# Optimization experiments

Measured on AMD Instinct MI355X. Metric: run time of the kernel, lower is better.

## Reference

```python
import jax, jax.numpy as jnp
import numpy as np

BATCH, H, NFAM = 32768, 1024, 10


def setup_inputs() -> dict:
    key = jax.random.key(0)
    k1, k2, k3, k4 = jax.random.split(key, 4)
    scale1 = 1.0 / np.sqrt(2 * H)
    scale2 = 1.0 / np.sqrt(H)
    return {
        "features": jax.random.normal(k1, (BATCH, H), dtype=jnp.float32),
        "prototypes": jax.random.normal(k2, (NFAM, H), dtype=jnp.float32),
        "W1": jax.random.normal(k3, (2 * H, H), dtype=jnp.float32) * scale1,
        "b1": jnp.zeros((H,), dtype=jnp.float32),
        "W2": jax.random.normal(k4, (H, H), dtype=jnp.float32) * scale2,
        "b2": jnp.zeros((H,), dtype=jnp.float32),
    }


def reference(features, prototypes, W1, b1, W2, b2):
    # Squared euclidean distances via the norm trick (avoids [B, NFAM, H] blowup).
    # argmin over squared distances == argmin over cdist (sqrt is monotone).
    f2 = jnp.sum(features * features, axis=1, keepdims=True)        # [B, 1]
    p2 = jnp.sum(prototypes * prototypes, axis=1)                   # [NFAM]
    d2 = f2 + p2[None, :] - 2.0 * (features @ prototypes.T)         # [B, NFAM]
    nearest_idx = jnp.argmin(d2, axis=1)                            # [B]
    nearest_prototypes = prototypes[nearest_idx]                    # [B, H]
    combined = jnp.concatenate([features, nearest_prototypes], axis=1)  # [B, 2H]
    hidden = jax.nn.relu(combined @ W1 + b1)                        # [B, H]
    adapted = hidden @ W2 + b2                                      # [B, H]
    return adapted
```

## Files before the change

### kernel.cpp

```cpp
#include <hip/hip_runtime.h>
#include <stdint.h>
#include <stddef.h>

#define BATCH 32768
#define HDIM  1024
#define NFAM  10

typedef short bf16x8 __attribute__((ext_vector_type(8)));
typedef float f32x4  __attribute__((ext_vector_type(4)));

__device__ __forceinline__ unsigned short f2bf(float x) {
  unsigned int u = __builtin_bit_cast(unsigned int, x);
  u += 0x7fffu + ((u >> 16) & 1u);
  return (unsigned short)(u >> 16);
}

__device__ __forceinline__ void async_cp16(unsigned short* lds_dst, const unsigned short* g_src) {
  __builtin_amdgcn_global_load_lds(
      (const __attribute__((address_space(1))) unsigned int*)g_src,
      (__attribute__((address_space(3))) unsigned int*)lds_dst,
      16, 0, 0);
}

__global__ __launch_bounds__(256) void transpose_cast(
    const float* __restrict__ in, unsigned short* __restrict__ out, int R, int C) {
  __shared__ float tile[64][65];
  const int t = threadIdx.x;
  const int c = t & 63;
  const int r0 = t >> 6;
  const int rbase = blockIdx.y * 64, cbase = blockIdx.x * 64;
#pragma unroll
  for (int i = 0; i < 16; ++i) {
    int r = r0 + i * 4;
    tile[r][c] = in[(size_t)(rbase + r) * C + cbase + c];
  }
  __syncthreads();
#pragma unroll
  for (int i = 0; i < 16; ++i) {
    int r = r0 + i * 4;
    out[(size_t)(cbase + r) * R + rbase + c] = f2bf(tile[c][r]);
  }
}

__global__ __launch_bounds__(256) void proto_prep(
    const float* __restrict__ protos, float* __restrict__ p2) {
  __shared__ float red[4];
  const int j = blockIdx.x, t = threadIdx.x;
  float4 v = ((const float4*)(protos + (size_t)j * HDIM))[t];
  float s = v.x * v.x + v.y * v.y + v.z * v.z + v.w * v.w;
#pragma unroll
  for (int o = 32; o > 0; o >>= 1) s += __shfl_down(s, o);
  if ((t & 63) == 0) red[t >> 6] = s;
  __syncthreads();
  if (t == 0) p2[j] = red[0] + red[1] + red[2] + red[3];
}

__global__ __launch_bounds__(256) void proto_contrib(
    const float* __restrict__ protos, const float* __restrict__ W1,
    const float* __restrict__ b1, float* __restrict__ protoC) {
  __shared__ float red[4][64];
  const int j  = blockIdx.y;
  const int ln = threadIdx.x & 63;
  const int ks = threadIdx.x >> 6;
  const int n  = blockIdx.x * 64 + ln;
  const float* p = protos + (size_t)j * HDIM + ks * 256;
  const float* w = W1 + (size_t)(HDIM + ks * 256) * HDIM + n;
  float s = 0.f;
#pragma unroll 16
  for (int kk = 0; kk < 256; ++kk)
    s += p[kk] * w[(size_t)kk * HDIM];
  red[ks][ln] = s;
  __syncthreads();
  if (ks == 0)
    protoC[j * HDIM + n] = red[0][ln] + red[1][ln] + red[2][ln] + red[3][ln] + b1[n];
}

__global__ __launch_bounds__(256) void nearest_kernel(
    const float* __restrict__ feats, const float* __restrict__ protos,
    const float* __restrict__ p2, unsigned short* __restrict__ featsB,
    int* __restrict__ idx) {
  __shared__ float pl[NFAM * HDIM];
  const int t = threadIdx.x;
#pragma unroll
  for (int j = 0; j < NFAM; ++j)
    ((float4*)pl)[t + 256 * j] = ((const float4*)protos)[t + 256 * j];
  __syncthreads();

  const int wave = t >> 6, lane = t & 63;
  float P2[NFAM];
#pragma unroll
  for (int j = 0; j < NFAM; ++j) P2[j] = p2[j];

#pragma unroll
  for (int rr = 0; rr < 4; ++rr) {
    const int row = blockIdx.x * 16 + wave * 4 + rr;
    const float* f = feats + (size_t)row * HDIM;

    float dot[NFAM];
#pragma unroll
    for (int j = 0; j < NFAM; ++j) dot[j] = 0.f;
    float f2 = 0.f;

#pragma unroll
    for (int ch = 0; ch < 4; ++ch) {
      const int k4 = ch * 64 + lane;
      float4 v = ((const float4*)f)[k4];
      f2 += v.x * v.x + v.y * v.y + v.z * v.z + v.w * v.w;
#pragma unroll
      for (int j = 0; j < NFAM; ++j) {
        float4 p = ((const float4*)pl)[j * 256 + k4];
        dot[j] += v.x * p.x + v.y * p.y + v.z * p.z + v.w * p.w;
      }
      uint2 pk;
      pk.x = (unsigned)f2bf(v.x) | ((unsigned)f2bf(v.y) << 16);
      pk.y = (unsigned)f2bf(v.z) | ((unsigned)f2bf(v.w) << 16);
      *(uint2*)(featsB + (size_t)row * HDIM + k4 * 4) = pk;
    }

#pragma unroll
    for (int o = 32; o > 0; o >>= 1) {
      f2 += __shfl_down(f2, o);
#pragma unroll
      for (int j = 0; j < NFAM; ++j) dot[j] += __shfl_down(dot[j], o);
    }
    if (lane == 0) {
      int best = 0;
      float bd = f2 + P2[0] - 2.f * dot[0];
#pragma unroll
      for (int j = 1; j < NFAM; ++j) {
        float d = f2 + P2[j] - 2.f * dot[j];
        if (d < bd) { bd = d; best = j; }
      }
      idx[row] = best;
    }
  }
}

template <int EPI>
__global__ __launch_bounds__(512, 2) void gemm256(
    const unsigned short* __restrict__ A,
    const unsigned short* __restrict__ Bt,
    const int* __restrict__ idx,
    const float* __restrict__ protoC,
    const float* __restrict__ bias,
    unsigned short* __restrict__ outB,
    float* __restrict__ outF) {
  constexpr int K  = 1024;
  constexpr int NT = K / 64;
  __shared__ unsigned short ldsA[2 * 2 * 2 * 128 * 32];
  __shared__ unsigned short ldsB[2 * 2 * 2 * 128 * 32];

  const int t    = threadIdx.x;
  const int lane = t & 63;
  const int quad = lane >> 4;
  const int r16  = lane & 15;
  const int wid  = t >> 6;
  const int wm   = wid >> 2;
  const int wn   = wid & 3;

  const int b = blockIdx.x;
  const int rowBase = ((b >> 5) + (b & 7) * 16) * 256;
  const int colBase = ((b >> 3) & 3) * 256;

  const int sr = t >> 2;
  const int q  = (t & 3) ^ ((t >> 3) & 3);
  const unsigned short* pA = A  + (size_t)(rowBase + sr) * K + q * 8;
  const unsigned short* pB = Bt + (size_t)(colBase + sr) * K + q * 8;
  const int ldst = t * 8;

  const int pr = quad ^ ((r16 >> 1) & 3);

  f32x4 acc[2][2][4][2];
#pragma unroll
  for (int a0 = 0; a0 < 2; ++a0)
#pragma unroll
    for (int b0 = 0; b0 < 2; ++b0)
#pragma unroll
      for (int m0 = 0; m0 < 4; ++m0)
#pragma unroll
        for (int n0 = 0; n0 < 2; ++n0) acc[a0][b0][m0][n0] = (f32x4){0.f, 0.f, 0.f, 0.f};

#define STAGE_A(buf, h, kb)                                                        \
  {                                                                                \
    async_cp16(ldsA + (buf) * 16384 + (0 * 2 + (h)) * 4096 + ldst,                 \
               pA + (size_t)(h) * (128 * K) + (kb) + 0 * 32);                      \
    async_cp16(ldsA + (buf) * 16384 + (1 * 2 + (h)) * 4096 + ldst,                 \
               pA + (size_t)(h) * (128 * K) + (kb) + 1 * 32);                      \
  }
#define STAGE_B(buf, h, kb)                                                        \
  {                                                                                \
    async_cp16(ldsB + (buf) * 16384 + (0 * 2 + (h)) * 4096 + ldst,                 \
               pB + (size_t)(h) * (128 * K) + (kb) + 0 * 32);                      \
    async_cp16(ldsB + (buf) * 16384 + (1 * 2 + (h)) * 4096 + ldst,                 \
               pB + (size_t)(h) * (128 * K) + (kb) + 1 * 32);                      \
  }
#define READ_A(dst, p_, h)                                                          \
  _Pragma("unroll")                                                                 \
  for (int s = 0; s < 2; ++s)                                                       \
    _Pragma("unroll")                                                               \
    for (int mi = 0; mi < 4; ++mi)                                                  \
      dst[s][mi] = *(const bf16x8*)(ldsA + (p_) * 16384 + (s * 2 + (h)) * 4096 +    \
                                    (wm * 64 + mi * 16 + r16) * 32 + pr * 8);
#define READ_B(dst, p_, h)                                                          \
  _Pragma("unroll")                                                                 \
  for (int s = 0; s < 2; ++s)                                                       \
    _Pragma("unroll")                                                               \
    for (int ni = 0; ni < 2; ++ni)                                                  \
      dst[s][ni] = *(const bf16x8*)(ldsB + (p_) * 16384 + (s * 2 + (h)) * 4096 +    \
                                    (wn * 32 + ni * 16 + r16) * 32 + pr * 8);
#define MFMA_Q(ah, bh, bsrc)                                                        \
  __builtin_amdgcn_s_setprio(1);                                                    \
  _Pragma("unroll")                                                                 \
  for (int s = 0; s < 2; ++s)                                                       \
    _Pragma("unroll")                                                               \
    for (int mi = 0; mi < 4; ++mi)                                                  \
      _Pragma("unroll")                                                             \
      for (int ni = 0; ni < 2; ++ni)                                                \
        acc[ah][bh][mi][ni] = __builtin_amdgcn_mfma_f32_16x16x32_bf16(              \
            av[s][mi], bsrc[s][ni], acc[ah][bh][mi][ni], 0, 0, 0);                  \
  __builtin_amdgcn_s_setprio(0);

  STAGE_A(0, 0, 0);
  STAGE_B(0, 1, 0);
  STAGE_A(0, 1, 0);
  STAGE_B(0, 0, 0);
  STAGE_A(1, 0, 64);
  STAGE_B(1, 1, 64);
  asm volatile("s_waitcnt vmcnt(4)" ::: "memory");
  __builtin_amdgcn_s_barrier();

  bf16x8 av[2][4], bvlo[2][2], bvhi[2][2];

  for (int kt = 0; kt < NT; ++kt) {
    const int p   = kt & 1;
    const int kb1 = ((kt + 1) & (NT - 1)) * 64;
    const int kb2 = ((kt + 2) & (NT - 1)) * 64;

    READ_A(av, p, 0);
    READ_B(bvlo, p, 0);
    STAGE_A(p ^ 1, 1, kb1);
    __builtin_amdgcn_s_barrier();
    MFMA_Q(0, 0, bvlo);
    __builtin_amdgcn_s_barrier();

    READ_B(bvhi, p, 1);
    STAGE_B(p ^ 1, 0, kb1);
    __builtin_amdgcn_s_barrier();
    MFMA_Q(0, 1, bvhi);
    __builtin_amdgcn_s_barrier();

    READ_A(av, p, 1);
    STAGE_A(p, 0, kb2);
    __builtin_amdgcn_s_barrier();
    MFMA_Q(1, 1, bvhi);
    __builtin_amdgcn_s_barrier();

    STAGE_B(p, 1, kb2);
    asm volatile("s_waitcnt vmcnt(4)" ::: "memory");
    __builtin_amdgcn_s_barrier();
    MFMA_Q(1, 0, bvlo);
    __builtin_amdgcn_s_barrier();
  }
#undef STAGE_A
#undef STAGE_B
#undef READ_A
#undef READ_B
#undef MFMA_Q

#pragma unroll
  for (int ah = 0; ah < 2; ++ah) {
#pragma unroll
    for (int mi = 0; mi < 4; ++mi) {
      const int grow0 = rowBase + ah * 128 + wm * 64 + mi * 16 + quad * 4;
      int pid[4];
      if (EPI) {
#pragma unroll
        for (int r = 0; r < 4; ++r) pid[r] = idx[grow0 + r];
      }
#pragma unroll
      for (int bh = 0; bh < 2; ++bh) {
#pragma unroll
        for (int ni = 0; ni < 2; ++ni) {
          const int gcol = colBase + bh * 128 + wn * 32 + ni * 16 + r16;
          if (EPI) {
#pragma unroll
            for (int r = 0; r < 4; ++r) {
              float v = acc[ah][bh][mi][ni][r] + protoC[(size_t)pid[r] * HDIM + gcol];
              v = fmaxf(v, 0.0f);
              outB[(size_t)(grow0 + r) * 1024 + gcol] = f2bf(v);
            }
          } else {
            const float bv = bias[gcol];
#pragma unroll
            for (int r = 0; r < 4; ++r)
              outF[(size_t)(grow0 + r) * 1024 + gcol] = acc[ah][bh][mi][ni][r] + bv;
          }
        }
      }
    }
  }
}

extern "C" void kernel_launch(void* const* d_in, const int* in_sizes, int n_in,
                              void* d_out, int out_size, void* d_ws, size_t ws_size,
                              hipStream_t stream) {
  const float* feats  = (const float*)d_in[0];
  const float* protos = (const float*)d_in[1];
  const float* W1     = (const float*)d_in[2];
  const float* b1     = (const float*)d_in[3];
  const float* W2     = (const float*)d_in[4];
  const float* b2     = (const float*)d_in[5];
  float* out = (float*)d_out;

  unsigned short* featsB  = (unsigned short*)d_ws;
  unsigned short* hiddenB = featsB + (size_t)BATCH * HDIM;
  unsigned short* W1t     = hiddenB + (size_t)BATCH * HDIM;
  unsigned short* W2t     = W1t + (size_t)HDIM * HDIM;
  float* protoC = (float*)(W2t + (size_t)HDIM * HDIM);
  float* p2     = protoC + NFAM * HDIM;
  int* idx      = (int*)(p2 + NFAM + 2);

  transpose_cast<<<dim3(HDIM / 64, HDIM / 64), 256, 0, stream>>>(W1, W1t, HDIM, HDIM);
  transpose_cast<<<dim3(HDIM / 64, HDIM / 64), 256, 0, stream>>>(W2, W2t, HDIM, HDIM);
  proto_prep<<<NFAM, 256, 0, stream>>>(protos, p2);
  proto_contrib<<<dim3(HDIM / 64, NFAM), 256, 0, stream>>>(protos, W1, b1, protoC);
  nearest_kernel<<<BATCH / 16, 256, 0, stream>>>(feats, protos, p2, featsB, idx);
  gemm256<1><<<512, 512, 0, stream>>>(featsB, W1t, idx, protoC, nullptr, hiddenB, nullptr);
  gemm256<0><<<512, 512, 0, stream>>>(hiddenB, W2t, nullptr, nullptr, b2, nullptr, out);
}
```

Baseline: 413.2 us.

## Merge five preprocessing kernels into one block-dispatched prep kernel

The two weight transpose-casts, prototype norm, prototype contribution and nearest-prototype kernels are merged into a single launch whose block index selects the role. Prototype squared norms are now computed redundantly inside each nearest block from LDS rather than by a separate kernel. This removes four launches and the serialization between independent small kernels, letting them overlap. In exchange, every block reserves the 40KB LDS sized for the largest role, which can reduce occupancy for the transpose and contrib blocks, and each nearest block does some extra reduction work.

Result: faster. 398.3 us (-3.6%).

```diff
diff --git a/kernel.cpp b/kernel.cpp
--- a/kernel.cpp
+++ b/kernel.cpp
@@ -22,117 +22,126 @@
       16, 0, 0);
 }
 
-__global__ __launch_bounds__(256) void transpose_cast(
-    const float* __restrict__ in, unsigned short* __restrict__ out, int R, int C) {
-  __shared__ float tile[64][65];
+#define NEAREST_BLKS  2048
+#define TR1_BASE      2048
+#define TR2_BASE      2304
+#define CONTRIB_BASE  2560
+#define PREP_BLKS     2720
+
+__global__ __launch_bounds__(256) void prep_kernel(
+    const float* __restrict__ feats, const float* __restrict__ protos,
+    const float* __restrict__ W1, const float* __restrict__ b1,
+    const float* __restrict__ W2,
+    unsigned short* __restrict__ featsB, int* __restrict__ idx,
+    float* __restrict__ protoC,
+    unsigned short* __restrict__ W1t, unsigned short* __restrict__ W2t) {
+  __shared__ __align__(16) char smem[40960];
+  const int b = blockIdx.x;
   const int t = threadIdx.x;
-  const int c = t & 63;
-  const int r0 = t >> 6;
-  const int rbase = blockIdx.y * 64, cbase = blockIdx.x * 64;
-#pragma unroll
-  for (int i = 0; i < 16; ++i) {
-    int r = r0 + i * 4;
-    tile[r][c] = in[(size_t)(rbase + r) * C + cbase + c];
-  }
-  __syncthreads();
-#pragma unroll
-  for (int i = 0; i < 16; ++i) {
-    int r = r0 + i * 4;
-    out[(size_t)(cbase + r) * R + rbase + c] = f2bf(tile[c][r]);
-  }
-}
-
-__global__ __launch_bounds__(256) void proto_prep(
-    const float* __restrict__ protos, float* __restrict__ p2) {
-  __shared__ float red[4];
-  const int j = blockIdx.x, t = threadIdx.x;
-  float4 v = ((const float4*)(protos + (size_t)j * HDIM))[t];
-  float s = v.x * v.x + v.y * v.y + v.z * v.z + v.w * v.w;
-#pragma unroll
-  for (int o = 32; o > 0; o >>= 1) s += __shfl_down(s, o);
-  if ((t & 63) == 0) red[t >> 6] = s;
-  __syncthreads();
-  if (t == 0) p2[j] = red[0] + red[1] + red[2] + red[3];
-}
-
-__global__ __launch_bounds__(256) void proto_contrib(
-    const float* __restrict__ protos, const float* __restrict__ W1,
-    const float* __restrict__ b1, float* __restrict__ protoC) {
-  __shared__ float red[4][64];
-  const int j  = blockIdx.y;
-  const int ln = threadIdx.x & 63;
-  const int ks = threadIdx.x >> 6;
-  const int n  = blockIdx.x * 64 + ln;
-  const float* p = protos + (size_t)j * HDIM + ks * 256;
-  const float* w = W1 + (size_t)(HDIM + ks * 256) * HDIM + n;
-  float s = 0.f;
+
+  if (b < NEAREST_BLKS) {
+    float* pl = (float*)smem;
+#pragma unroll
+    for (int j = 0; j < NFAM; ++j)
+      ((float4*)pl)[t + 256 * j] = ((const float4*)protos)[t + 256 * j];
+    __syncthreads();
+
+    const int wave = t >> 6, lane = t & 63;
+
+    float P2[NFAM];
+#pragma unroll
+    for (int j = 0; j < NFAM; ++j) {
+      float s = 0.f;
+#pragma unroll
+      for (int c = 0; c < 4; ++c) {
+        float4 v = ((const float4*)pl)[j * 256 + c * 64 + lane];
+        s += v.x * v.x + v.y * v.y + v.z * v.z + v.w * v.w;
+      }
+#pragma unroll
+      for (int o = 32; o > 0; o >>= 1) s += __shfl_down(s, o);
+      P2[j] = s;
+    }
+
+#pragma unroll
+    for (int rr = 0; rr < 4; ++rr) {
+      const int row = b * 16 + wave * 4 + rr;
+      const float* f = feats + (size_t)row * HDIM;
+
+      float dot[NFAM];
+#pragma unroll
+      for (int j = 0; j < NFAM; ++j) dot[j] = 0.f;
+      float f2 = 0.f;
+
+#pragma unroll
+      for (int ch = 0; ch < 4; ++ch) {
+        const int k4 = ch * 64 + lane;
+        float4 v = ((const float4*)f)[k4];
+        f2 += v.x * v.x + v.y * v.y + v.z * v.z + v.w * v.w;
+#pragma unroll
+        for (int j = 0; j < NFAM; ++j) {
+          float4 p = ((const float4*)pl)[j * 256 + k4];
+          dot[j] += v.x * p.x + v.y * p.y + v.z * p.z + v.w * p.w;
+        }
+        uint2 pk;
+        pk.x = (unsigned)f2bf(v.x) | ((unsigned)f2bf(v.y) << 16);
+        pk.y = (unsigned)f2bf(v.z) | ((unsigned)f2bf(v.w) << 16);
+        *(uint2*)(featsB + (size_t)row * HDIM + k4 * 4) = pk;
+      }
+
+#pragma unroll
+      for (int o = 32; o > 0; o >>= 1) {
+        f2 += __shfl_down(f2, o);
+#pragma unroll
+        for (int j = 0; j < NFAM; ++j) dot[j] += __shfl_down(dot[j], o);
+      }
+      if (lane == 0) {
+        int best = 0;
+        float bd = f2 + P2[0] - 2.f * dot[0];
+#pragma unroll
+        for (int j = 1; j < NFAM; ++j) {
+          float d = f2 + P2[j] - 2.f * dot[j];
+          if (d < bd) { bd = d; best = j; }
+        }
+        idx[row] = best;
+      }
+    }
+  } else if (b < CONTRIB_BASE) {
+    const int bi = (b < TR2_BASE) ? (b - TR1_BASE) : (b - TR2_BASE);
+    const float* in = (b < TR2_BASE) ? W1 : W2;
+    unsigned short* out = (b < TR2_BASE) ? W1t : W2t;
+    float (*tile)[65] = (float(*)[65])smem;
+    const int c = t & 63;
+    const int r0 = t >> 6;
+    const int rbase = (bi >> 4) * 64, cbase = (bi & 15) * 64;
+#pragma unroll
+    for (int i = 0; i < 16; ++i) {
+      int r = r0 + i * 4;
+      tile[r][c] = in[(size_t)(rbase + r) * HDIM + cbase + c];
+    }
+    __syncthreads();
+#pragma unroll
+    for (int i = 0; i < 16; ++i) {
+      int r = r0 + i * 4;
+      out[(size_t)(cbase + r) * HDIM + rbase + c] = f2bf(tile[c][r]);
+    }
+  } else {
+    float (*red)[64] = (float(*)[64])smem;
+    const int bi = b - CONTRIB_BASE;
+    const int j  = bi >> 4;
+    const int nc = bi & 15;
+    const int ln = t & 63;
+    const int ks = t >> 6;
+    const int n  = nc * 64 + ln;
+    const float* p = protos + (size_t)j * HDIM + ks * 256;
+    const float* w = W1 + (size_t)(HDIM + ks * 256) * HDIM + n;
+    float s = 0.f;
 #pragma unroll 16
-  for (int kk = 0; kk < 256; ++kk)
-    s += p[kk] * w[(size_t)kk * HDIM];
-  red[ks][ln] = s;
-  __syncthreads();
-  if (ks == 0)
-    protoC[j * HDIM + n] = red[0][ln] + red[1][ln] + red[2][ln] + red[3][ln] + b1[n];
-}
-
-__global__ __launch_bounds__(256) void nearest_kernel(
-    const float* __restrict__ feats, const float* __restrict__ protos,
-    const float* __restrict__ p2, unsigned short* __restrict__ featsB,
-    int* __restrict__ idx) {
-  __shared__ float pl[NFAM * HDIM];
-  const int t = threadIdx.x;
-#pragma unroll
-  for (int j = 0; j < NFAM; ++j)
-    ((float4*)pl)[t + 256 * j] = ((const float4*)protos)[t + 256 * j];
-  __syncthreads();
-
-  const int wave = t >> 6, lane = t & 63;
-  float P2[NFAM];
-#pragma unroll
-  for (int j = 0; j < NFAM; ++j) P2[j] = p2[j];
-
-#pragma unroll
-  for (int rr = 0; rr < 4; ++rr) {
-    const int row = blockIdx.x * 16 + wave * 4 + rr;
-    const float* f = feats + (size_t)row * HDIM;
-
-    float dot[NFAM];
-#pragma unroll
-    for (int j = 0; j < NFAM; ++j) dot[j] = 0.f;
-    float f2 = 0.f;
-
-#pragma unroll
-    for (int ch = 0; ch < 4; ++ch) {
-      const int k4 = ch * 64 + lane;
-      float4 v = ((const float4*)f)[k4];
-      f2 += v.x * v.x + v.y * v.y + v.z * v.z + v.w * v.w;
-#pragma unroll
-      for (int j = 0; j < NFAM; ++j) {
-        float4 p = ((const float4*)pl)[j * 256 + k4];
-        dot[j] += v.x * p.x + v.y * p.y + v.z * p.z + v.w * p.w;
-      }
-      uint2 pk;
-      pk.x = (unsigned)f2bf(v.x) | ((unsigned)f2bf(v.y) << 16);
-      pk.y = (unsigned)f2bf(v.z) | ((unsigned)f2bf(v.w) << 16);
-      *(uint2*)(featsB + (size_t)row * HDIM + k4 * 4) = pk;
-    }
-
-#pragma unroll
-    for (int o = 32; o > 0; o >>= 1) {
-      f2 += __shfl_down(f2, o);
-#pragma unroll
-      for (int j = 0; j < NFAM; ++j) dot[j] += __shfl_down(dot[j], o);
-    }
-    if (lane == 0) {
-      int best = 0;
-      float bd = f2 + P2[0] - 2.f * dot[0];
-#pragma unroll
-      for (int j = 1; j < NFAM; ++j) {
-        float d = f2 + P2[j] - 2.f * dot[j];
-        if (d < bd) { bd = d; best = j; }
-      }
-      idx[row] = best;
-    }
+    for (int kk = 0; kk < 256; ++kk)
+      s += p[kk] * w[(size_t)kk * HDIM];
+    red[ks][ln] = s;
+    __syncthreads();
+    if (ks == 0)
+      protoC[j * HDIM + n] = red[0][ln] + red[1][ln] + red[2][ln] + red[3][ln] + b1[n];
   }
 }
 
@@ -317,14 +326,10 @@
   unsigned short* W1t     = hiddenB + (size_t)BATCH * HDIM;
   unsigned short* W2t     = W1t + (size_t)HDIM * HDIM;
   float* protoC = (float*)(W2t + (size_t)HDIM * HDIM);
-  float* p2     = protoC + NFAM * HDIM;
-  int* idx      = (int*)(p2 + NFAM + 2);
-
-  transpose_cast<<<dim3(HDIM / 64, HDIM / 64), 256, 0, stream>>>(W1, W1t, HDIM, HDIM);
-  transpose_cast<<<dim3(HDIM / 64, HDIM / 64), 256, 0, stream>>>(W2, W2t, HDIM, HDIM);
-  proto_prep<<<NFAM, 256, 0, stream>>>(protos, p2);
-  proto_contrib<<<dim3(HDIM / 64, NFAM), 256, 0, stream>>>(protos, W1, b1, protoC);
-  nearest_kernel<<<BATCH / 16, 256, 0, stream>>>(feats, protos, p2, featsB, idx);
+  int* idx      = (int*)(protoC + NFAM * HDIM);
+
+  prep_kernel<<<PREP_BLKS, 256, 0, stream>>>(
+      feats, protos, W1, b1, W2, featsB, idx, protoC, W1t, W2t);
   gemm256<1><<<512, 512, 0, stream>>>(featsB, W1t, idx, protoC, nullptr, hiddenB, nullptr);
   gemm256<0><<<512, 512, 0, stream>>>(hiddenB, W2t, nullptr, nullptr, b2, nullptr, out);
 }
```
